# Performance work log

Measured on AMD Instinct MI355X. Metric: run time of the kernel, lower is better.

## Reference

```python
import jax, jax.numpy as jnp
import numpy as np

MEAN_DEG = 3.8
QS = (2, 4, 8, 16, 32, 64)
POOL_DIM = 100
BP_ITERS = 10


def _bn(x, g, b):
    # BatchNorm1d in training mode: biased batch statistics over the node dim
    m = x.mean(0)
    v = ((x - m) ** 2).mean(0)
    return g * (x - m) * jax.lax.rsqrt(v + 1e-5) + b


def _gcn_sparse(x, src, dst, n, w, b):
    # GCNConv: add self loops, symmetric deg^-1/2 normalization, scatter-add aggregation
    loop = jnp.arange(n, dtype=src.dtype)
    s2 = jnp.concatenate([src, loop])
    d2 = jnp.concatenate([dst, loop])
    deg = jax.ops.segment_sum(jnp.ones(s2.shape[0], x.dtype), d2, num_segments=n)
    dinv = jnp.where(deg > 0, jax.lax.rsqrt(deg), 0.0)
    norm = (dinv[s2] * dinv[d2])[:, None]
    return jax.ops.segment_sum((x @ w)[s2] * norm, d2, num_segments=n) + b


def _gcn_dense(x, adj, w, b):
    # GCN on the dense pooled adjacency (pooled graphs are fully connected)
    n = adj.shape[-1]
    A = adj + jnp.eye(n, dtype=adj.dtype)
    d = A.sum(-1)
    dinv = jnp.where(d > 0, jax.lax.rsqrt(d), 0.0)
    An = dinv[:, :, None] * A * dinv[:, None, :]
    return jnp.einsum('bij,bjd->bid', An, x @ w) + b


def _bp(src, dst, n, q, beta, seed):
    # SBM-style belief propagation: iterate node marginals psi [n,q] for a fixed
    # number of sweeps; coupling exp(beta), global external field ~ mean_degree.
    key = jax.random.fold_in(jax.random.key(42), seed)
    psi0 = jax.nn.softmax(jax.random.normal(key, (n, q), jnp.float32), -1)
    eb = jnp.expm1(beta)

    def step(psi, _):
        msg = jax.ops.segment_sum(jnp.log1p(eb * psi[src]), dst, num_segments=n)
        field = (MEAN_DEG * beta / n) * psi.sum(0)
        return jax.nn.softmax(msg - field, -1), None

    psi, _ = jax.lax.scan(step, psi0, None, length=BP_ITERS)
    return psi


def _forward(x, w11, b11, g11, be11, w12, b12, g12, be12, w13, b13, g13, be13,
             bp_betas, pool_w, pool_b,
             w21, b21, g21, be21, w22, b22, g22, be22, w23, b23, g23, be23,
             fc1_w, fc1_b, fc2_w, fc2_b, edge_index, num_graphs):
    n = x.shape[0]
    B = num_graphs
    N = n // B
    src, dst = edge_index[0], edge_index[1]
    # per-graph dense adjacency (edge_index_to_csr -> todense, duplicates sum)
    adj = jnp.zeros((B, N, N), x.dtype).at[src // N, src % N, dst % N].add(1.0)

    # stage 1: three GCN + BN layers on the raw graph
    x11 = _bn(_gcn_sparse(x, src, dst, n, w11, b11), g11, be11)
    x12 = _bn(_gcn_sparse(x11, src, dst, n, w12, b12), g12, be12)
    x13 = _bn(_gcn_sparse(x12, src, dst, n, w13, b13), g13, be13)
    x1_out = jnp.concatenate([x11, x12, x13], -1).reshape(B, N, -1).max(1)  # [B,90]

    # six belief-propagation runs -> concat assignments [n, 2+4+...+64 = 126]
    s1 = jnp.concatenate([_bp(src, dst, n, q, bp_betas[i], i) for i, q in enumerate(QS)], -1)
    s1 = s1 @ pool_w + pool_b  # [n, 100]

    # dense diff-pool
    s1 = jax.nn.softmax(s1.reshape(B, N, POOL_DIM), -1)
    p1_x = jnp.einsum('bnk,bnd->bkd', s1, x13.reshape(B, N, -1))   # [B,100,30]
    p1_adj = jnp.einsum('bnk,bnm,bml->bkl', s1, adj, s1)           # [B,100,100]

    # stage 2: three dense GCN + BN layers on pooled graphs
    C = 30
    x21 = _bn(_gcn_dense(p1_x, p1_adj, w21, b21).reshape(-1, C), g21, be21)
    x22 = _bn(_gcn_dense(x21.reshape(B, POOL_DIM, C), p1_adj, w22, b22).reshape(-1, C), g22, be22)
    x23 = _bn(_gcn_dense(x22.reshape(B, POOL_DIM, C), p1_adj, w23, b23).reshape(-1, C), g23, be23)
    x2_out = jnp.concatenate([x21, x22, x23], -1).reshape(B, POOL_DIM, -1).max(1)  # [B,90]

    conv_out = jnp.concatenate([x1_out, x2_out], -1)  # [B,180]
    out = jax.nn.relu(conv_out @ fc1_w + fc1_b) @ fc2_w + fc2_b  # dropout p=0 -> identity
    return out, jnp.zeros((1,), x.dtype)


def setup_inputs() -> dict:
    key = jax.random.key(0)
    B, N, EP = 64, 1024, 8192
    ks = jax.random.split(key, 24)
    x = jax.random.normal(ks[0], (B * N, 3), jnp.float32)
    off = (jnp.arange(B, dtype=jnp.int32) * N)[:, None]
    src = (jax.random.randint(ks[1], (B, EP), 0, N, jnp.int32) + off).reshape(-1)
    dst = (jax.random.randint(ks[2], (B, EP), 0, N, jnp.int32) + off).reshape(-1)
    edge_index = jnp.stack([src, dst])

    def lin(k, i, o):
        return jax.random.normal(k, (i, o), jnp.float32) / np.sqrt(i)

    p = {}
    dims1 = [(3, 30), (30, 30), (30, 30)]
    for idx, (i, o) in enumerate(dims1, 1):
        p['w1%d' % idx] = lin(ks[2 + idx], i, o)
        p['b1%d' % idx] = jnp.zeros((o,), jnp.float32)
        p['g1%d' % idx] = jnp.ones((o,), jnp.float32)
        p['be1%d' % idx] = jnp.zeros((o,), jnp.float32)
    for idx in (1, 2, 3):
        p['w2%d' % idx] = lin(ks[8 + idx], 30, 30)
        p['b2%d' % idx] = jnp.zeros((30,), jnp.float32)
        p['g2%d' % idx] = jnp.ones((30,), jnp.float32)
        p['be2%d' % idx] = jnp.zeros((30,), jnp.float32)
    qs = np.array(QS, np.float32)
    p['bp_betas'] = jnp.asarray(np.log(qs / (np.sqrt(MEAN_DEG) - 1.0) + 1.0))
    p['pool_w'] = lin(ks[15], 126, 100); p['pool_b'] = jnp.zeros((100,), jnp.float32)
    p['fc1_w'] = lin(ks[16], 180, 50); p['fc1_b'] = jnp.zeros((50,), jnp.float32)
    p['fc2_w'] = lin(ks[17], 50, 6); p['fc2_b'] = jnp.zeros((6,), jnp.float32)
    return {'x': x, 'edge_index': edge_index, 'num_graphs': B, **p}


def reference(x, edge_index, num_graphs, w11, b11, g11, be11, w12, b12, g12, be12,
              w13, b13, g13, be13, bp_betas, pool_w, pool_b,
              w21, b21, g21, be21, w22, b22, g22, be22, w23, b23, g23, be23,
              fc1_w, fc1_b, fc2_w, fc2_b):
    return _forward(x, w11, b11, g11, be11, w12, b12, g12, be12, w13, b13, g13, be13,
                    bp_betas, pool_w, pool_b,
                    w21, b21, g21, be21, w22, b22, g22, be22, w23, b23, g23, be23,
                    fc1_w, fc1_b, fc2_w, fc2_b, edge_index, num_graphs)
```

## Files before the change

### kernel.cpp

```cpp
#include <hip/hip_runtime.h>
#include <stdint.h>
#include <float.h>


constexpr int NN    = 65536;
constexpr int NEDGE = 524288;
constexpr int NBG   = 64;

__constant__ int cQS[6]   = {2,4,8,16,32,64};

__device__ __forceinline__ void tf2x32(uint32_t k0, uint32_t k1, uint32_t x0, uint32_t x1,
                                       uint32_t& o0, uint32_t& o1){
  uint32_t ks[3] = {k0, k1, k0 ^ k1 ^ 0x1BD11BDAu};
  x0 += ks[0]; x1 += ks[1];
  const int RA[4] = {13,15,26,6}, RB[4] = {17,29,16,24};
  #pragma unroll
  for (int i=0;i<5;i++){
    const int* r = (i&1)? RB : RA;
    #pragma unroll
    for (int j=0;j<4;j++){
      x0 += x1;
      x1 = (x1 << r[j]) | (x1 >> (32 - r[j]));
      x1 ^= x0;
    }
// ... 126 lines not shown
                                              float* __restrict__ h, int nrow){
  __shared__ float ws[CIN*30];
  int t = threadIdx.x;
  for (int i=t;i<CIN*30;i+=256) ws[i] = w[i];
  __syncthreads();
  int id = blockIdx.x*256 + t;
  if (id >= nrow*30) return;
  int v = id/30, j = id - v*30;
  const float* xr = x + v*CIN;
  float acc = 0.f;
  #pragma unroll
  for (int k=0;k<CIN;k++) acc += xr[k]*ws[k*30+j];
  h[id] = acc;
}

__global__ __launch_bounds__(256) void k_mm30c(const float* __restrict__ x, const float* __restrict__ wfold,
                                               const float* __restrict__ cvec, float* __restrict__ h, int nrow){
  __shared__ float ws[900];
  __shared__ float cl[30];
  int t = threadIdx.x;
  for (int i=t;i<900;i+=256) ws[i] = wfold[i];
  if (t < 30) cl[t] = cvec[t];
  __syncthreads();
  int id = blockIdx.x*256 + t;
  if (id >= nrow*30) return;
  int v = id/30, j = id - v*30;
  const float* xr = x + v*30;
  float acc = cl[j];
  #pragma unroll
  for (int k=0;k<30;k++) acc += xr[k]*ws[k*30+j];
  h[id] = acc;
}

__global__ __launch_bounds__(256) void k_gcn_agg(const float* __restrict__ h, const int* __restrict__ rp,
    const int* __restrict__ col, const float* __restrict__ dinv, const float* __restrict__ bias,
    float* __restrict__ y, float* __restrict__ gS, float* __restrict__ gQ){
  __shared__ float binS[30], binQ[30];
  int t = threadIdx.x;
  if (t < 30){ binS[t]=0.f; binQ[t]=0.f; }
  __syncthreads();
  int b = blockIdx.x;
  int xcd = b & 7, i = b >> 3;
  int gs = i/60, j = i - gs*60;
  int graph = gs*8 + xcd;
  int idwg = j*256 + t;
  int rw = idwg/15, pr = idwg - rw*15;
  int v = graph*1024 + rw;
  float dv = dinv[v];
  float accx = 0.f, accy = 0.f;
  int a = rp[v], e = rp[v+1];
  for (; a+4<=e; a+=4){
    int s0=col[a], s1=col[a+1], s2=col[a+2], s3=col[a+3];
    float d0=dinv[s0], d1=dinv[s1], d2=dinv[s2], d3=dinv[s3];
    float2 h0=*(const float2*)(h+s0*30+2*pr), h1=*(const float2*)(h+s1*30+2*pr);
    float2 h2=*(const float2*)(h+s2*30+2*pr), h3=*(const float2*)(h+s3*30+2*pr);
    accx += h0.x*(d0*dv); accy += h0.y*(d0*dv);
    accx += h1.x*(d1*dv); accy += h1.y*(d1*dv);
    accx += h2.x*(d2*dv); accy += h2.y*(d2*dv);
    accx += h3.x*(d3*dv); accy += h3.y*(d3*dv);
  }
  for (; a<e; ++a){
    int s = col[a];
    float w = dinv[s]*dv;
    float2 hv = *(const float2*)(h+s*30+2*pr);
    accx += hv.x*w; accy += hv.y*w;
  }
  float2 hs = *(const float2*)(h + v*30 + 2*pr);
  float w2 = dv*dv;
  accx += hs.x*w2; accy += hs.y*w2;
  float2 o; o.x = accx + bias[2*pr]; o.y = accy + bias[2*pr+1];
  *(float2*)(y + v*30 + 2*pr) = o;
  atomicAdd(&binS[2*pr],   o.x); atomicAdd(&binQ[2*pr],   o.x*o.x);
  atomicAdd(&binS[2*pr+1], o.y); atomicAdd(&binQ[2*pr+1], o.y*o.y);
  __syncthreads();
  if (t < 30){
    int slot = (b & 63)*30 + t;
    atomicAdd(&gS[slot], binS[t]);
    atomicAdd(&gQ[slot], binQ[t]);
  }
}

template<int FOLD>
__global__ __launch_bounds__(256) void k_bnw(float* __restrict__ gS, float* __restrict__ gQ, float n,
    const float* __restrict__ g, const float* __restrict__ be,
    const float* __restrict__ wnext, float* __restrict__ sfc,
    float* __restrict__ wfold, float* __restrict__ cvec){
  __shared__ float s_l[30], c_l[30];
  int t = threadIdx.x;
  if (t < 30){
    float s=0.f, q=0.f;
    for (int u=0;u<64;u++){ s += gS[u*30+t]; q += gQ[u*30+t]; }
    float m = s/n;
    float var = q/n - m*m;
    float sc = g[t]*(1.0f/sqrtf(var+1e-5f));
    float c0 = be[t] - sc*m;
    s_l[t]=sc; c_l[t]=c0;
    sfc[t]=sc; sfc[32+t]=c0;
    for (int u=0;u<64;u++){ gS[u*30+t]=0.f; gQ[u*30+t]=0.f; }
  }
  __syncthreads();
  if (FOLD){
    for (int i=t;i<900;i+=256) wfold[i] = s_l[i/30]*wnext[i];
    if (t<30){
      float c=0.f;
      for (int k=0;k<30;k++) c += c_l[k]*wnext[k*30+t];
      cvec[t]=c;
    }
  }
}

__device__ __forceinline__ void bp_decode2(int b, int& graph, int& run, int& jj){
  int xcd = b & 7, i = b >> 3;
  int gs = i >> 7, j = i & 127;
  if      (j <   4){ run=0; jj=j;    }
// ... 58 lines not shown
    float m0=fmaxf(z[0],z[1]), m1=fmaxf(z[1],z[0]);
    float e0=expf(z[0]-m0), e1=expf(z[1]-m1);
    float s0=e0+e1, s1=e1+e0;
    float p0=e0/s0, p1=e1/s1;
    ((float2*)(psi_pk + (size_t)NN*CO))[row] = make_float2(p0,p1);
    ((float2*)(lg     + (size_t)NN*CO))[row] = make_float2(log1pf(eb*p0), log1pf(eb*p1));
  } else {
    int rw = idx >> L2T, ct = idx & (TPR-1);
    int row = graph*1024 + rw;
    float z[4];
    #pragma unroll
    for (int r=0;r<4;r++){
      uint32_t b0,b1;
      tf2x32(k0,k1, 0u, (uint32_t)(row*Q + 4*ct + r), b0,b1);
      uint32_t bits = b0 ^ b1;
      float f = __uint_as_float((bits>>9) | 0x3F800000u) - 1.0f;
      const float lo = __uint_as_float(0xBF7FFFFFu);
      float u = fmaxf(lo, f*2.0f + lo);
      z[r] = __uint_as_float(0x3FB504F3u) * erfinv32(u);
    }
    float m0=z[0],m1=z[1],m2=z[2],m3=z[3];
    bfly_max4<TPR>(m0,m1,m2,m3);
    float e0=expf(z[0]-m0), e1=expf(z[1]-m1), e2=expf(z[2]-m2), e3=expf(z[3]-m3);
    float s0=e0,s1=e1,s2=e2,s3=e3;
    bfly_sum4<TPR>(s0,s1,s2,s3);
    float p0=e0/s0, p1=e1/s1, p2=e2/s2, p3=e3/s3;
    ((float4*)(psi_pk + (size_t)NN*CO))[(size_t)row*TPR + ct] = make_float4(p0,p1,p2,p3);
    ((float4*)(lg     + (size_t)NN*CO))[(size_t)row*TPR + ct] =
        make_float4(log1pf(eb*p0), log1pf(eb*p1), log1pf(eb*p2), log1pf(eb*p3));
  }
}

__global__ __launch_bounds__(256) void k_bp_first(float* __restrict__ psi_pk, float* __restrict__ lg,
                                                  const float* __restrict__ betas){
  int graph, run, jj;
  bp_decode2(blockIdx.x, graph, run, jj);
  uint32_t k0, k1;
  tf2x32(0u, 42u, 0u, (uint32_t)run, k0, k1);
  float eb = expm1f(betas[run]);
  switch(run){
    case 0: bp_first_elem2< 2, 0, 1,0>(graph, jj, psi_pk, lg, eb, k0, k1); break;
    case 1: bp_first_elem2< 4, 2, 1,0>(graph, jj, psi_pk, lg, eb, k0, k1); break;
    case 2: bp_first_elem2< 8, 6, 2,1>(graph, jj, psi_pk, lg, eb, k0, k1); break;
    case 3: bp_first_elem2<16,14, 4,2>(graph, jj, psi_pk, lg, eb, k0, k1); break;
    case 4: bp_first_elem2<32,30, 8,3>(graph, jj, psi_pk, lg, eb, k0, k1); break;
    default:bp_first_elem2<64,62,16,4>(graph, jj, psi_pk, lg, eb, k0, k1); break;
  }
}

template<int Q, int CO, int TPR, int L2T>
__device__ __forceinline__ void bp_step_elem2(int graph, int run, int jj,
    const float* __restrict__ lcur, float* __restrict__ nxt, float* __restrict__ lnxt,
    const int* __restrict__ rp, const int* __restrict__ col,
    const float* __restrict__ field, float eb, int fin){
  int idx = jj*256 + (int)threadIdx.x;
  if constexpr (Q == 2){
    int row = graph*1024 + idx;
    const float2* B2 = (const float2*)(lcur + (size_t)NN*CO);
    float a0=0.f, a1=0.f;
    int a = rp[row], b2 = rp[row+1];
    for (; a+8<=b2; a+=8){
      int s0=col[a],s1=col[a+1],s2=col[a+2],s3=col[a+3];
      int s4=col[a+4],s5=col[a+5],s6=col[a+6],s7=col[a+7];
      float2 u0=B2[s0], u1=B2[s1], u2=B2[s2], u3=B2[s3];
      float2 u4=B2[s4], u5=B2[s5], u6=B2[s6], u7=B2[s7];
      a0+=u0.x; a1+=u0.y; a0+=u1.x; a1+=u1.y;
      a0+=u2.x; a1+=u2.y; a0+=u3.x; a1+=u3.y;
// ... 47 lines not shown
      float4 u0=B4[(size_t)s0*TPR+ct], u1=B4[(size_t)s1*TPR+ct];
      float4 u2=B4[(size_t)s2*TPR+ct], u3=B4[(size_t)s3*TPR+ct];
      a0+=u0.x; a1+=u0.y; a2+=u0.z; a3+=u0.w;
      a0+=u1.x; a1+=u1.y; a2+=u1.z; a3+=u1.w;
      a0+=u2.x; a1+=u2.y; a2+=u2.z; a3+=u2.w;
      a0+=u3.x; a1+=u3.y; a2+=u3.z; a3+=u3.w;
    }
    for (; a<b2; ++a){
      float4 u = B4[(size_t)col[a]*TPR+ct];
      a0+=u.x; a1+=u.y; a2+=u.z; a3+=u.w;
    }
    const float4 fld = *(const float4*)(field + run*64 + 4*ct);
    float v0 = a0 - fld.x, v1 = a1 - fld.y, v2 = a2 - fld.z, v3 = a3 - fld.w;
    float m0=v0,m1=v1,m2=v2,m3=v3;
    bfly_max4<TPR>(m0,m1,m2,m3);
    float e0=expf(v0-m0), e1=expf(v1-m1), e2=expf(v2-m2), e3=expf(v3-m3);
    float s0=e0,s1=e1,s2=e2,s3=e3;
    bfly_sum4<TPR>(s0,s1,s2,s3);
    float p0=e0/s0, p1=e1/s1, p2=e2/s2, p3=e3/s3;
    if (fin){
      float* o = nxt + (size_t)row*126 + CO + 4*ct;
      o[0]=p0; o[1]=p1; o[2]=p2; o[3]=p3;
    } else {
      ((float4*)(nxt  + (size_t)NN*CO))[(size_t)row*TPR+ct] = make_float4(p0,p1,p2,p3);
      ((float4*)(lnxt + (size_t)NN*CO))[(size_t)row*TPR+ct] =
          make_float4(log1pf(eb*p0), log1pf(eb*p1), log1pf(eb*p2), log1pf(eb*p3));
    }
  }
}

__global__ __launch_bounds__(256) void k_bp_step(
    float* __restrict__ nxt, const float* __restrict__ lcur, float* __restrict__ lnxt,
    const int* __restrict__ rp, const int* __restrict__ col,
    const float* __restrict__ field, const float* __restrict__ betas, int fin){
  int graph, run, jj;
  bp_decode2(blockIdx.x, graph, run, jj);
  float eb = expm1f(betas[run]);
  switch(run){
    case 0: bp_step_elem2< 2, 0, 1,0>(graph, run, jj, lcur, nxt, lnxt, rp, col, field, eb, fin); break;
    case 1: bp_step_elem2< 4, 2, 1,0>(graph, run, jj, lcur, nxt, lnxt, rp, col, field, eb, fin); break;
    case 2: bp_step_elem2< 8, 6, 2,1>(graph, run, jj, lcur, nxt, lnxt, rp, col, field, eb, fin); break;
    case 3: bp_step_elem2<16,14, 4,2>(graph, run, jj, lcur, nxt, lnxt, rp, col, field, eb, fin); break;
    case 4: bp_step_elem2<32,30, 8,3>(graph, run, jj, lcur, nxt, lnxt, rp, col, field, eb, fin); break;
    default:bp_step_elem2<64,62,16,4>(graph, run, jj, lcur, nxt, lnxt, rp, col, field, eb, fin); break;
  }
}

__global__ __launch_bounds__(64) void k_colsum_part(const float* __restrict__ psi_pk, float* __restrict__ part){
  int b = blockIdx.x;
  int xcd = b & 7, i = b >> 3;
  int gs = i/24, rem = i - gs*24;
  int run = rem >> 2, cg = rem & 3;
  int graph = gs*8 + xcd;
  int chunk = graph*4 + cg;
  int q = cQS[run];
  int co = (run==0)?0:(run==1)?2:(run==2)?6:(run==3)?14:(run==4)?30:62;
  int c = threadIdx.x;
  if (q >= 4){
    int nq = q >> 2;
    if (c >= nq) return;
    const float4* p4 = (const float4*)(psi_pk + (size_t)NN*co + (size_t)chunk*256*q) + c;
    float s0=0.f,s1=0.f,s2=0.f,s3=0.f;
    #pragma unroll 8
    for (int r=0;r<256;r++){
      float4 u = p4[(size_t)r*nq];
      s0+=u.x; s1+=u.y; s2+=u.z; s3+=u.w;
    }
    float* o = part + (run*256 + chunk)*64 + 4*c;
    o[0]=s0; o[1]=s1; o[2]=s2; o[3]=s3;
  } else {
    if (c >= q) return;
    float s = 0.f;
    const float* p = psi_pk + (size_t)NN*co + (size_t)chunk*256*q + c;
    #pragma unroll 8
    for (int r=0;r<256;r++) s += p[r*q];
    part[(run*256 + chunk)*64 + c] = s;
  }
}

__global__ void k_field(const float* __restrict__ part, const float* __restrict__ betas,
                        float* __restrict__ field){
  int id = threadIdx.x;
  int run = id >> 6, c = id & 63;
  if (c >= cQS[run]) return;
  float s = 0.f;
  for (int b=0;b<256;b++) s += part[(run*256 + b)*64 + c];
  float beta = betas[run];
  field[id] = s * (3.8f*beta/65536.0f);
}

__global__ __launch_bounds__(256) void k_catT(const float* __restrict__ cat, float* __restrict__ catT){
  __shared__ float tile[64*127];
  int b = blockIdx.x, t = threadIdx.x;
  const float* src = cat + (size_t)b*64*126;
  for (int i=t;i<8064;i+=256){
    int r = i/126, k = i - r*126;
    tile[r*127 + k] = src[i];
  }
  __syncthreads();
  for (int i=t;i<8064;i+=256){
    int k = i>>6, r = i&63;
    catT[(size_t)k*65536 + b*64 + r] = tile[r*127 + k];
  }
}

__global__ __launch_bounds__(256) void k_s1t(const float* __restrict__ catT, const float* __restrict__ pw,
                                             const float* __restrict__ pb, float* __restrict__ s1){
  __shared__ float wl[12600];
  __shared__ float pbl[100];
  __shared__ float redM[2][128];
  __shared__ float redS[2][128];
  int t = threadIdx.x;
  for (int i=t;i<12600;i+=256) wl[i] = pw[i];
  if (t < 100) pbl[t] = pb[t];
// ... 49 lines not shown
  int a = rp[v], e = rp[v+1];
  for (; a+8<=e; a+=8){
    int s0=col[a], s1_=col[a+1], s2=col[a+2], s3=col[a+3];
    int s4=col[a+4], s5=col[a+5], s6=col[a+6], s7=col[a+7];
    float4 u0=S4[(size_t)s0*25+quad], u1=S4[(size_t)s1_*25+quad];
    float4 u2=S4[(size_t)s2*25+quad], u3=S4[(size_t)s3*25+quad];
    float4 u4=S4[(size_t)s4*25+quad], u5=S4[(size_t)s5*25+quad];
    float4 u6=S4[(size_t)s6*25+quad], u7=S4[(size_t)s7*25+quad];
    a0+=u0.x; a1+=u0.y; a2+=u0.z; a3+=u0.w;
    a0+=u1.x; a1+=u1.y; a2+=u1.z; a3+=u1.w;
    a0+=u2.x; a1+=u2.y; a2+=u2.z; a3+=u2.w;
    a0+=u3.x; a1+=u3.y; a2+=u3.z; a3+=u3.w;
    a0+=u4.x; a1+=u4.y; a2+=u4.z; a3+=u4.w;
    a0+=u5.x; a1+=u5.y; a2+=u5.z; a3+=u5.w;
    a0+=u6.x; a1+=u6.y; a2+=u6.z; a3+=u6.w;
    a0+=u7.x; a1+=u7.y; a2+=u7.z; a3+=u7.w;
  }
  for (; a+4<=e; a+=4){
    int s0=col[a], s1_=col[a+1], s2=col[a+2], s3=col[a+3];
    float4 u0=S4[(size_t)s0*25+quad], u1=S4[(size_t)s1_*25+quad];
    float4 u2=S4[(size_t)s2*25+quad], u3=S4[(size_t)s3*25+quad];
    a0+=u0.x; a1+=u0.y; a2+=u0.z; a3+=u0.w;
    a0+=u1.x; a1+=u1.y; a2+=u1.z; a3+=u1.w;
    a0+=u2.x; a1+=u2.y; a2+=u2.z; a3+=u2.w;
    a0+=u3.x; a1+=u3.y; a2+=u3.z; a3+=u3.w;
  }
  for (; a<e; ++a){
    float4 u = S4[(size_t)col[a]*25+quad];
    a0+=u.x; a1+=u.y; a2+=u.z; a3+=u.w;
  }
  ((float4*)T)[(size_t)v*25 + quad] = make_float4(a0,a1,a2,a3);
}

__global__ __launch_bounds__(512) void k_p1adj_sk(const float* __restrict__ s1, const float* __restrict__ T,
                                                  float* __restrict__ part){
  __shared__ float sS[6400];
  __shared__ float sT[6400];
  int blk = blockIdx.x;
  int b = blk >> 2, qtr = blk & 3;
  int t = threadIdx.x;
  int tk = t/20, tl = t - tk*20;
  bool act = t < 500;
  int k0 = tk*4, l0 = tl*5;
  float acc[4][5];
  #pragma unroll
  for (int i=0;i<4;i++)
    #pragma unroll
    for (int j=0;j<5;j++) acc[i][j] = 0.f;
  const float* s1b = s1 + (size_t)b*102400;
  const float* Tb  = T  + (size_t)b*102400;
  for (int c=qtr*4; c<qtr*4+4; c++){
    for (int i=t;i<6400;i+=512){ sS[i] = s1b[c*6400+i]; sT[i] = Tb[c*6400+i]; }
    __syncthreads();
    if (act){
      #pragma unroll 2
      for (int n=0;n<64;n++){
        const float* sr = &sS[n*100 + k0];
        const float* tr = &sT[n*100 + l0];
        float s0=sr[0], s1v=sr[1], s2=sr[2], s3=sr[3];
        float t0=tr[0], t1=tr[1], t2=tr[2], t3=tr[3], t4=tr[4];
        acc[0][0]+=s0*t0; acc[0][1]+=s0*t1; acc[0][2]+=s0*t2; acc[0][3]+=s0*t3; acc[0][4]+=s0*t4;
        acc[1][0]+=s1v*t0; acc[1][1]+=s1v*t1; acc[1][2]+=s1v*t2; acc[1][3]+=s1v*t3; acc[1][4]+=s1v*t4;
        acc[2][0]+=s2*t0; acc[2][1]+=s2*t1; acc[2][2]+=s2*t2; acc[2][3]+=s2*t3; acc[2][4]+=s2*t4;
        acc[3][0]+=s3*t0; acc[3][1]+=s3*t1; acc[3][2]+=s3*t2; acc[3][3]+=s3*t3; acc[3][4]+=s3*t4;
      }
    }
    __syncthreads();
  }
  if (act){
    float* pp = part + (size_t)qtr*640000 + (size_t)b*10000;
    #pragma unroll
    for (int i=0;i<4;i++){
      float* o = pp + (k0+i)*100 + l0;
      #pragma unroll
      for (int j=0;j<5;j++) o[j] = acc[i][j];
    }
  }
}

__global__ __launch_bounds__(256) void k_p1x_sk(const float* __restrict__ s1, const float* __restrict__ y3,
                                                const float* __restrict__ sfc, float* __restrict__ part){
  __shared__ float sS[6400];
  __shared__ float sX[1920];
  int blk = blockIdx.x;
  int b = blk >> 2, qtr = blk & 3;
  int t = threadIdx.x;
  int tk = t/10, tl = t - tk*10;
  bool act = t < 250;
  int k0 = tk*4, d0 = tl*3;
  float acc[4][3];
  #pragma unroll
  for (int i=0;i<4;i++)
    #pragma unroll
    for (int j=0;j<3;j++) acc[i][j] = 0.f;
  const float* s1b = s1 + (size_t)b*102400;
  const float* xb  = y3 + (size_t)b*30720;
  for (int c=qtr*4; c<qtr*4+4; c++){
    for (int i=t;i<6400;i+=256) sS[i] = s1b[c*6400+i];
    for (int i=t;i<1920;i+=256){
      int f = i % 30;
      sX[i] = sfc[f]*xb[c*1920+i] + sfc[32+f];
    }
    __syncthreads();
    if (act){
      #pragma unroll 2
      for (int n=0;n<64;n++){
        const float* sr = &sS[n*100 + k0];
        const float* xr = &sX[n*30 + d0];
        float s0=sr[0], s1v=sr[1], s2=sr[2], s3=sr[3];
        float x0=xr[0], x1=xr[1], x2=xr[2];
        acc[0][0]+=s0*x0; acc[0][1]+=s0*x1; acc[0][2]+=s0*x2;
        acc[1][0]+=s1v*x0; acc[1][1]+=s1v*x1; acc[1][2]+=s1v*x2;
        acc[2][0]+=s2*x0; acc[2][1]+=s2*x1; acc[2][2]+=s2*x2;
        acc[3][0]+=s3*x0; acc[3][1]+=s3*x1; acc[3][2]+=s3*x2;
      }
    }
    __syncthreads();
  }
  if (act){
    float* pp = part + (size_t)qtr*192000 + (size_t)b*3000;
    #pragma unroll
    for (int i=0;i<4;i++){
      float* o = pp + (k0+i)*30 + d0;
      #pragma unroll
      for (int j=0;j<3;j++) o[j] = acc[i][j];
    }
  }
}

__global__ __launch_bounds__(256) void k_ppred(const float* __restrict__ partA, const float* __restrict__ partX,
                                               float* __restrict__ padj, float* __restrict__ px){
  int id = blockIdx.x*256 + threadIdx.x;
  if (id < 640000){
    float s = partA[id] + partA[640000+id] + partA[1280000+id] + partA[1920000+id];
    padj[id] = s;
  } else if (id < 832000){
    int j = id - 640000;
    float s = partX[j] + partX[192000+j] + partX[384000+j] + partX[576000+j];
    px[j] = s;
  }
}

__global__ __launch_bounds__(256) void k_An1(const float* __restrict__ padj, float* __restrict__ An){
  __shared__ float dv[100];
  int b = blockIdx.x, t = threadIdx.x;
  if (t < 100){
    const float* r = padj + (size_t)b*10000 + t*100;
    float s = 0.f;
    for (int l=0;l<100;l++){
      float v = r[l];
      if (l==t) v += 1.0f;
      s += v;
    }
    dv[t] = 1.0f/sqrtf(s);
  }
  __syncthreads();
  for (int i=t;i<10000;i+=256){
    int k = i/100, l = i - k*100;
    float a = padj[(size_t)b*10000 + i] + ((k==l)? 1.0f : 0.0f);
    An[(size_t)b*10000 + i] = (dv[k]*a)*dv[l];
  }
}

__global__ __launch_bounds__(256) void k_y2(const float* __restrict__ An, const float* __restrict__ h,
    const float* __restrict__ bias, float* __restrict__ y,
    float* __restrict__ gS, float* __restrict__ gQ){
  __shared__ float binS[30], binQ[30];
  int t = threadIdx.x;
  if (t < 30){ binS[t]=0.f; binQ[t]=0.f; }
  __syncthreads();
  int id = blockIdx.x*256 + t;
  float val = 0.f;
  int d = 0;
  if (id < NBG*100*30){
    d = id % 30;
    int bk = id / 30;
    int b = bk / 100;
    const float* Ar = An + bk*100;
    const float* hb = h + b*100*30;
    float acc = 0.f;
    for (int l=0;l<100;l++) acc += Ar[l]*hb[l*30+d];
    val = acc + bias[d];
    y[id] = val;
    atomicAdd(&binS[d], val);
    atomicAdd(&binQ[d], val*val);
  }
  __syncthreads();
  if (t < 30){
    int slot = (blockIdx.x & 63)*30 + t;
    atomicAdd(&gS[slot], binS[t]);
    atomicAdd(&gQ[slot], binQ[t]);
  }
}

__global__ __launch_bounds__(256) void k_pool2(const float* __restrict__ A,
    const float* __restrict__ Bv, const float* __restrict__ Cv,
    const float* __restrict__ sfcBase,
    int rows, float* __restrict__ conv, int coff){
  __shared__ float lds[256*31];
  int b = blockIdx.x, a = blockIdx.y, t = threadIdx.x;
  const float* X = (a==0)? A : ((a==1)? Bv : Cv);
  const float* sf = sfcBase + a*64;
  float acc[30];
  #pragma unroll
  for (int f=0;f<30;f++) acc[f] = -FLT_MAX;
  for (int r=t; r<rows; r+=256){
    const float* xr = X + (size_t)(b*rows + r)*30;
    #pragma unroll
    for (int f=0;f<30;f++) acc[f] = fmaxf(acc[f], sf[f]*xr[f] + sf[32+f]);
  }
  #pragma unroll
  for (int f=0;f<30;f++) lds[t*31+f] = acc[f];
  __syncthreads();
  for (int s=128;s>0;s>>=1){
    if (t<s){
// ... 50 lines not shown
  uint8_t* basep = (uint8_t*)d_ws;
  size_t off = 0;
  auto take = [&](size_t bytes)->void*{
    void* p = basep + off;
    off = (off + bytes + 255) & ~(size_t)255;
    return p;
  };
  int* degi    = (int*)take((size_t)NN*4);
  int* dego    = (int*)take((size_t)NN*4);
  int* cntA    = (int*)take((size_t)NN*4);
  int* cntB    = (int*)take((size_t)NN*4);
  float* gS    = (float*)take(64*30*4);
  float* gQ    = (float*)take(64*30*4);
  int* rp_in   = (int*)take((size_t)(NN+1)*4);
  int* rp_out  = (int*)take((size_t)(NN+1)*4);
  int* bsum    = (int*)take(512*4);
  int* col_in  = (int*)take((size_t)NEDGE*4);
  int* col_out = (int*)take((size_t)NEDGE*4);
  float* dinv  = (float*)take((size_t)NN*4);
  float* hbuf  = (float*)take((size_t)NN*30*4);
  float* X1    = (float*)take((size_t)NN*30*4);
  float* X2    = (float*)take((size_t)NN*30*4);
  float* X3    = (float*)take((size_t)NN*30*4);
  float* bufA  = (float*)take((size_t)NN*126*4);
  float* bufB  = (float*)take((size_t)NN*126*4);
  float* logA  = (float*)take((size_t)NN*126*4);
  float* logB  = (float*)take((size_t)NN*126*4);
  float* partCS= (float*)take((size_t)6*256*64*4);
  float* fieldv= (float*)take(384*4);
  float* sfcAll= (float*)take(6*64*4);
  float* wfold = (float*)take(960*4);
  float* cvec  = (float*)take(32*4);
  float* px    = (float*)take(192000*4);
  float* padj  = (float*)take(640000*4);
  float* An    = (float*)take(640000*4);
  float* h2    = (float*)take(192000*4);
  float* X21   = (float*)take(192000*4);
  float* X22   = (float*)take(192000*4);
  float* X23   = (float*)take(192000*4);
  float* conv  = (float*)take(64*180*4);

  float* catT     = logA;
  float* pAdjPart = logB;
  float* pPxPart  = logB + 2560000;

  hipMemsetAsync(degi, 0, (size_t)4*NN*4 + 2*64*30*4, stream);
  k_count<<<2048,256,0,stream>>>(src,dst,degi,dego);
  k_scan1<<<dim3(256,2),256,0,stream>>>(degi, dego, rp_in, rp_out, bsum);
  k_scan2<<<2,256,0,stream>>>(bsum);
  k_scan3<<<dim3(256,2),256,0,stream>>>(rp_in, rp_out, bsum);
  k_fill<<<dim3(2048,2),256,0,stream>>>(src, dst, rp_in, rp_out, cntA, cntB, col_in, col_out);
  k_sortrow<<<dim3(256,2),256,0,stream>>>(rp_in, rp_out, col_in, col_out, src, dst, degi, dinv);

  k_mm30<3><<<7680,256,0,stream>>>(x, w11, hbuf, NN);
  k_gcn_agg<<<3840,256,0,stream>>>(hbuf, rp_in, col_in, dinv, b11, X1, gS, gQ);
  k_bnw<1><<<1,256,0,stream>>>(gS, gQ, 65536.f, g11, be11, w12, sfcAll+0*64, wfold, cvec);
  k_mm30c<<<7680,256,0,stream>>>(X1, wfold, cvec, hbuf, NN);
  k_gcn_agg<<<3840,256,0,stream>>>(hbuf, rp_in, col_in, dinv, b12, X2, gS, gQ);
  k_bnw<1><<<1,256,0,stream>>>(gS, gQ, 65536.f, g12, be12, w13, sfcAll+1*64, wfold, cvec);
  k_mm30c<<<7680,256,0,stream>>>(X2, wfold, cvec, hbuf, NN);
  k_gcn_agg<<<3840,256,0,stream>>>(hbuf, rp_in, col_in, dinv, b13, X3, gS, gQ);
  k_bnw<0><<<1,256,0,stream>>>(gS, gQ, 65536.f, g13, be13, nullptr, sfcAll+2*64, nullptr, nullptr);
  k_pool2<<<dim3(NBG,3),256,0,stream>>>(X1, X2, X3, sfcAll, 1024, conv, 0);

  k_bp_first<<<8192,256,0,stream>>>(bufA, logA, betas);
  float* cur = bufA;  float* nxt = bufB;
  float* lcur = logA; float* lnxt = logB;
  for (int it=0; it<10; ++it){
    k_colsum_part<<<1536,64,0,stream>>>(cur, partCS);
    k_field<<<1,384,0,stream>>>(partCS, betas, fieldv);
    int fin = (it==9);
    k_bp_step<<<8192,256,0,stream>>>(nxt, lcur, lnxt, rp_in, col_in, fieldv, betas, fin);
    float* tp = cur;  cur = nxt;   nxt = tp;
    float* tl = lcur; lcur = lnxt; lnxt = tl;
  }

  k_catT<<<1024,256,0,stream>>>(bufA, catT);
  k_s1t<<<512,256,0,stream>>>(catT, poolw, poolb, bufB);
  k_T<<<6400,256,0,stream>>>(bufB, rp_out, col_out, bufA);
  k_p1adj_sk<<<256,512,0,stream>>>(bufB, bufA, pAdjPart);
  k_p1x_sk<<<256,256,0,stream>>>(bufB, X3, sfcAll+2*64, pPxPart);
  k_ppred<<<3250,256,0,stream>>>(pAdjPart, pPxPart, padj, px);
  k_An1<<<64,256,0,stream>>>(padj, An);

  k_mm30<30><<<750,256,0,stream>>>(px, w21, h2, NBG*100);
  k_y2<<<750,256,0,stream>>>(An, h2, b21, X21, gS, gQ);
  k_bnw<1><<<1,256,0,stream>>>(gS, gQ, 6400.f, g21, be21, w22, sfcAll+3*64, wfold, cvec);
  k_mm30c<<<750,256,0,stream>>>(X21, wfold, cvec, h2, NBG*100);
  k_y2<<<750,256,0,stream>>>(An, h2, b22, X22, gS, gQ);
  k_bnw<1><<<1,256,0,stream>>>(gS, gQ, 6400.f, g22, be22, w23, sfcAll+4*64, wfold, cvec);
  k_mm30c<<<750,256,0,stream>>>(X22, wfold, cvec, h2, NBG*100);
  k_y2<<<750,256,0,stream>>>(An, h2, b23, X23, gS, gQ);
  k_bnw<0><<<1,256,0,stream>>>(gS, gQ, 6400.f, g23, be23, nullptr, sfcAll+5*64, nullptr, nullptr);
  k_pool2<<<dim3(NBG,3),256,0,stream>>>(X21, X22, X23, sfcAll+3*64, 100, conv, 90);

  k_fc<<<64,64,0,stream>>>(conv, fc1w, fc1b, fc2w, fc2b, out);
}
```

Measured before the change: 1.288 ms.

## Overlap first-stage GCN layers with BP sweeps via auxiliary blocks in shared launches

Moves the independent first-stage GCN work (linear transforms, sparse aggregation, BN statistics folding and max-pooling) into extra blocks appended to the BP kernel launches, so those stages run alongside the BP iterations instead of as separate serial launches. The BN fold is carried as a second block of k_field. The pooled-adjacency and pooled-feature partial GEMMs are merged into one launch, and the partial-sum reduction is fused with the An normalisation. This cuts launch count and serial dependency chains, at the cost of heavier, divergent kernels with more shared memory and a hand-tracked dependency schedule across iterations.

Result: faster. 1.235 ms, median of 2 (-4.1%).

```diff
diff --git a/kernel.cpp b/kernel.cpp
--- a/kernel.cpp
+++ b/kernel.cpp
@@ -182,54 +182,6 @@
   h[id] = acc;
 }
 
-__global__ __launch_bounds__(256) void k_gcn_agg(const float* __restrict__ h, const int* __restrict__ rp,
-    const int* __restrict__ col, const float* __restrict__ dinv, const float* __restrict__ bias,
-    float* __restrict__ y, float* __restrict__ gS, float* __restrict__ gQ){
-  __shared__ float binS[30], binQ[30];
-  int t = threadIdx.x;
-  if (t < 30){ binS[t]=0.f; binQ[t]=0.f; }
-  __syncthreads();
-  int b = blockIdx.x;
-  int xcd = b & 7, i = b >> 3;
-  int gs = i/60, j = i - gs*60;
-  int graph = gs*8 + xcd;
-  int idwg = j*256 + t;
-  int rw = idwg/15, pr = idwg - rw*15;
-  int v = graph*1024 + rw;
-  float dv = dinv[v];
-  float accx = 0.f, accy = 0.f;
-  int a = rp[v], e = rp[v+1];
-  for (; a+4<=e; a+=4){
-    int s0=col[a], s1=col[a+1], s2=col[a+2], s3=col[a+3];
-    float d0=dinv[s0], d1=dinv[s1], d2=dinv[s2], d3=dinv[s3];
-    float2 h0=*(const float2*)(h+s0*30+2*pr), h1=*(const float2*)(h+s1*30+2*pr);
-    float2 h2=*(const float2*)(h+s2*30+2*pr), h3=*(const float2*)(h+s3*30+2*pr);
-    accx += h0.x*(d0*dv); accy += h0.y*(d0*dv);
-    accx += h1.x*(d1*dv); accy += h1.y*(d1*dv);
-    accx += h2.x*(d2*dv); accy += h2.y*(d2*dv);
-    accx += h3.x*(d3*dv); accy += h3.y*(d3*dv);
-  }
-  for (; a<e; ++a){
-    int s = col[a];
-    float w = dinv[s]*dv;
-    float2 hv = *(const float2*)(h+s*30+2*pr);
-    accx += hv.x*w; accy += hv.y*w;
-  }
-  float2 hs = *(const float2*)(h + v*30 + 2*pr);
-  float w2 = dv*dv;
-  accx += hs.x*w2; accy += hs.y*w2;
-  float2 o; o.x = accx + bias[2*pr]; o.y = accy + bias[2*pr+1];
-  *(float2*)(y + v*30 + 2*pr) = o;
-  atomicAdd(&binS[2*pr],   o.x); atomicAdd(&binQ[2*pr],   o.x*o.x);
-  atomicAdd(&binS[2*pr+1], o.y); atomicAdd(&binQ[2*pr+1], o.y*o.y);
-  __syncthreads();
-  if (t < 30){
-    int slot = (b & 63)*30 + t;
-    atomicAdd(&gS[slot], binS[t]);
-    atomicAdd(&gQ[slot], binQ[t]);
-  }
-}
-
 template<int FOLD>
 __global__ __launch_bounds__(256) void k_bnw(float* __restrict__ gS, float* __restrict__ gQ, float n,
     const float* __restrict__ g, const float* __restrict__ be,
@@ -354,7 +306,25 @@
 }
 
 __global__ __launch_bounds__(256) void k_bp_first(float* __restrict__ psi_pk, float* __restrict__ lg,
-                                                  const float* __restrict__ betas){
+                                                  const float* __restrict__ betas,
+                                                  const float* __restrict__ xin,
+                                                  const float* __restrict__ w11,
+                                                  float* __restrict__ hbuf){
+  if (blockIdx.x >= 8192){
+    __shared__ float ws[90];
+    int t = threadIdx.x;
+    for (int i=t;i<90;i+=256) ws[i] = w11[i];
+    __syncthreads();
+    int id = ((int)blockIdx.x - 8192)*256 + t;
+    if (id >= NN*30) return;
+    int v = id/30, j = id - v*30;
+    const float* xr = xin + v*3;
+    float acc = 0.f;
+    #pragma unroll
+    for (int k=0;k<3;k++) acc += xr[k]*ws[k*30+j];
+    hbuf[id] = acc;
+    return;
+  }
   int graph, run, jj;
   bp_decode2(blockIdx.x, graph, run, jj);
   uint32_t k0, k1;
@@ -468,7 +438,101 @@
 __global__ __launch_bounds__(256) void k_bp_step(
     float* __restrict__ nxt, const float* __restrict__ lcur, float* __restrict__ lnxt,
     const int* __restrict__ rp, const int* __restrict__ col,
-    const float* __restrict__ field, const float* __restrict__ betas, int fin){
+    const float* __restrict__ field, const float* __restrict__ betas, int fin,
+    int auxType, const float* __restrict__ aA, const float* __restrict__ aB,
+    const float* __restrict__ aC, float* __restrict__ aO,
+    float* __restrict__ agS, float* __restrict__ agQ,
+    const float* __restrict__ adinv, const float* __restrict__ asfc,
+    float* __restrict__ aconv){
+  if (blockIdx.x >= 8192){
+    __shared__ float smem[960];
+    int ab = (int)blockIdx.x - 8192;
+    int t = threadIdx.x;
+    if (auxType == 1){
+      float* binS = smem; float* binQ = smem + 32;
+      if (t < 30){ binS[t]=0.f; binQ[t]=0.f; }
+      __syncthreads();
+      int xcd = ab & 7, i = ab >> 3;
+      int gs = i/60, j = i - gs*60;
+      int graph = gs*8 + xcd;
+      int idwg = j*256 + t;
+      int rw = idwg/15, pr = idwg - rw*15;
+      int v = graph*1024 + rw;
+      float dv = adinv[v];
+      float accx = 0.f, accy = 0.f;
+      int a = rp[v], e = rp[v+1];
+      for (; a+4<=e; a+=4){
+        int s0=col[a], s1=col[a+1], s2=col[a+2], s3=col[a+3];
+        float d0=adinv[s0], d1=adinv[s1], d2=adinv[s2], d3=adinv[s3];
+        float2 h0=*(const float2*)(aA+s0*30+2*pr), h1=*(const float2*)(aA+s1*30+2*pr);
+        float2 h2=*(const float2*)(aA+s2*30+2*pr), h3=*(const float2*)(aA+s3*30+2*pr);
+        accx += h0.x*(d0*dv); accy += h0.y*(d0*dv);
+        accx += h1.x*(d1*dv); accy += h1.y*(d1*dv);
+        accx += h2.x*(d2*dv); accy += h2.y*(d2*dv);
+        accx += h3.x*(d3*dv); accy += h3.y*(d3*dv);
+      }
+      for (; a<e; ++a){
+        int s = col[a];
+        float w = adinv[s]*dv;
+        float2 hv = *(const float2*)(aA+s*30+2*pr);
+        accx += hv.x*w; accy += hv.y*w;
+      }
+      float2 hs = *(const float2*)(aA + v*30 + 2*pr);
+      float w2 = dv*dv;
+      accx += hs.x*w2; accy += hs.y*w2;
+      float2 o; o.x = accx + aB[2*pr]; o.y = accy + aB[2*pr+1];
+      *(float2*)(aO + v*30 + 2*pr) = o;
+      atomicAdd(&binS[2*pr],   o.x); atomicAdd(&binQ[2*pr],   o.x*o.x);
+      atomicAdd(&binS[2*pr+1], o.y); atomicAdd(&binQ[2*pr+1], o.y*o.y);
+      __syncthreads();
+      if (t < 30){
+        int slot = (ab & 63)*30 + t;
+        atomicAdd(&agS[slot], binS[t]);
+        atomicAdd(&agQ[slot], binQ[t]);
+      }
+    } else if (auxType == 2){
+      float* ws = smem; float* cl = smem + 904;
+      for (int i=t;i<900;i+=256) ws[i] = aB[i];
+      if (t < 30) cl[t] = aC[t];
+      __syncthreads();
+      int id = ab*256 + t;
+      if (id < NN*30){
+        int v = id/30, j = id - v*30;
+        const float* xr = aA + v*30;
+        float acc = cl[j];
+        #pragma unroll
+        for (int k=0;k<30;k++) acc += xr[k]*ws[k*30+j];
+        aO[id] = acc;
+      }
+    } else if (auxType == 3){
+      int b2 = ab & 63, a = ab >> 6;
+      const float* X = (a==0)? aA : ((a==1)? aB : aC);
+      const float* sf = asfc + a*64;
+      float acc[30];
+      #pragma unroll
+      for (int f=0;f<30;f++) acc[f] = -FLT_MAX;
+      for (int r=t; r<1024; r+=256){
+        const float* xr = X + (size_t)(b2*1024 + r)*30;
+        #pragma unroll
+        for (int f=0;f<30;f++) acc[f] = fmaxf(acc[f], sf[f]*xr[f] + sf[32+f]);
+      }
+      #pragma unroll
+      for (int off=32; off; off>>=1){
+        #pragma unroll
+        for (int f=0;f<30;f++) acc[f] = fmaxf(acc[f], __shfl_xor(acc[f], off, 64));
+      }
+      int w = t>>6, lane = t&63;
+      if (lane == 0){
+        #pragma unroll
+        for (int f=0;f<30;f++) smem[w*30+f] = acc[f];
+      }
+      __syncthreads();
+      if (t < 30)
+        aconv[b2*180 + a*30 + t] =
+          fmaxf(fmaxf(smem[t], smem[30+t]), fmaxf(smem[60+t], smem[90+t]));
+    }
+    return;
+  }
   int graph, run, jj;
   bp_decode2(blockIdx.x, graph, run, jj);
   float eb = expm1f(betas[run]);
@@ -515,7 +579,37 @@
 }
 
 __global__ void k_field(const float* __restrict__ part, const float* __restrict__ betas,
-                        float* __restrict__ field){
+                        float* __restrict__ field,
+                        int auxFold, float* __restrict__ gS, float* __restrict__ gQ, float n,
+                        const float* __restrict__ g, const float* __restrict__ be,
+                        const float* __restrict__ wnext, float* __restrict__ sfc,
+                        float* __restrict__ wfold, float* __restrict__ cvec){
+  if (blockIdx.x == 1){
+    if (auxFold < 0) return;
+    __shared__ float s_l[30], c_l[30];
+    int t = threadIdx.x;
+    if (t < 30){
+      float s=0.f, q=0.f;
+      for (int u=0;u<64;u++){ s += gS[u*30+t]; q += gQ[u*30+t]; }
+      float m = s/n;
+      float var = q/n - m*m;
+      float sc = g[t]*(1.0f/sqrtf(var+1e-5f));
+      float c0 = be[t] - sc*m;
+      s_l[t]=sc; c_l[t]=c0;
+      sfc[t]=sc; sfc[32+t]=c0;
+      for (int u=0;u<64;u++){ gS[u*30+t]=0.f; gQ[u*30+t]=0.f; }
+    }
+    __syncthreads();
+    if (auxFold == 1){
+      for (int i=t;i<900;i+=384) wfold[i] = s_l[i/30]*wnext[i];
+      if (t<30){
+        float c=0.f;
+        for (int k=0;k<30;k++) c += c_l[k]*wnext[k*30+t];
+        cvec[t]=c;
+      }
+    }
+    return;
+  }
   int id = threadIdx.x;
   int run = id >> 6, c = id & 63;
   if (c >= cQS[run]) return;
@@ -631,133 +725,130 @@
   ((float4*)T)[(size_t)v*25 + quad] = make_float4(a0,a1,a2,a3);
 }
 
-__global__ __launch_bounds__(512) void k_p1adj_sk(const float* __restrict__ s1, const float* __restrict__ T,
-                                                  float* __restrict__ part){
+__global__ __launch_bounds__(512) void k_p1ax(const float* __restrict__ s1, const float* __restrict__ T,
+                                              const float* __restrict__ y3, const float* __restrict__ sfc,
+                                              float* __restrict__ partA, float* __restrict__ partX){
   __shared__ float sS[6400];
   __shared__ float sT[6400];
-  int blk = blockIdx.x;
-  int b = blk >> 2, qtr = blk & 3;
   int t = threadIdx.x;
-  int tk = t/20, tl = t - tk*20;
-  bool act = t < 500;
-  int k0 = tk*4, l0 = tl*5;
-  float acc[4][5];
-  #pragma unroll
-  for (int i=0;i<4;i++)
+  if (blockIdx.x < 256){
+    int blk = blockIdx.x;
+    int b = blk >> 2, qtr = blk & 3;
+    int tk = t/20, tl = t - tk*20;
+    bool act = t < 500;
+    int k0 = tk*4, l0 = tl*5;
+    float acc[4][5];
     #pragma unroll
-    for (int j=0;j<5;j++) acc[i][j] = 0.f;
-  const float* s1b = s1 + (size_t)b*102400;
-  const float* Tb  = T  + (size_t)b*102400;
-  for (int c=qtr*4; c<qtr*4+4; c++){
-    for (int i=t;i<6400;i+=512){ sS[i] = s1b[c*6400+i]; sT[i] = Tb[c*6400+i]; }
+    for (int i=0;i<4;i++)
+      #pragma unroll
+      for (int j=0;j<5;j++) acc[i][j] = 0.f;
+    const float* s1b = s1 + (size_t)b*102400;
+    const float* Tb  = T  + (size_t)b*102400;
+    for (int c=qtr*4; c<qtr*4+4; c++){
+      for (int i=t;i<6400;i+=512){ sS[i] = s1b[c*6400+i]; sT[i] = Tb[c*6400+i]; }
+      __syncthreads();
+      if (act){
+        #pragma unroll 2
+        for (int n=0;n<64;n++){
+          const float* sr = &sS[n*100 + k0];
+          const float* tr = &sT[n*100 + l0];
+          float s0=sr[0], s1v=sr[1], s2=sr[2], s3=sr[3];
+          float t0=tr[0], t1=tr[1], t2=tr[2], t3=tr[3], t4=tr[4];
+          acc[0][0]+=s0*t0; acc[0][1]+=s0*t1; acc[0][2]+=s0*t2; acc[0][3]+=s0*t3; acc[0][4]+=s0*t4;
+          acc[1][0]+=s1v*t0; acc[1][1]+=s1v*t1; acc[1][2]+=s1v*t2; acc[1][3]+=s1v*t3; acc[1][4]+=s1v*t4;
+          acc[2][0]+=s2*t0; acc[2][1]+=s2*t1; acc[2][2]+=s2*t2; acc[2][3]+=s2*t3; acc[2][4]+=s2*t4;
+          acc[3][0]+=s3*t0; acc[3][1]+=s3*t1; acc[3][2]+=s3*t2; acc[3][3]+=s3*t3; acc[3][4]+=s3*t4;
+        }
+      }
+      __syncthreads();
+    }
+    if (act){
+      float* pp = partA + (size_t)qtr*640000 + (size_t)b*10000;
+      #pragma unroll
+      for (int i=0;i<4;i++){
+        float* o = pp + (k0+i)*100 + l0;
+        #pragma unroll
+        for (int j=0;j<5;j++) o[j] = acc[i][j];
+      }
+    }
+  } else {
+    int blk = blockIdx.x - 256;
+    int b = blk >> 2, qtr = blk & 3;
+    float* sX = sT;
+    int tk = t/10, tl = t - tk*10;
+    bool act = t < 250;
+    int k0 = tk*4, d0 = tl*3;
+    float acc[4][3];
+    #pragma unroll
+    for (int i=0;i<4;i++)
+      #pragma unroll
+      for (int j=0;j<3;j++) acc[i][j] = 0.f;
+    const float* s1b = s1 + (size_t)b*102400;
+    const float* xb  = y3 + (size_t)b*30720;
+    for (int c=qtr*4; c<qtr*4+4; c++){
+      for (int i=t;i<6400;i+=512) sS[i] = s1b[c*6400+i];
+      for (int i=t;i<1920;i+=512){
+        int f = i % 30;
+        sX[i] = sfc[f]*xb[c*1920+i] + sfc[32+f];
+      }
+      __syncthreads();
+      if (act){
+        #pragma unroll 2
+        for (int n=0;n<64;n++){
+          const float* sr = &sS[n*100 + k0];
+          const float* xr = &sX[n*30 + d0];
+          float s0=sr[0], s1v=sr[1], s2=sr[2], s3=sr[3];
+          float x0=xr[0], x1=xr[1], x2=xr[2];
+          acc[0][0]+=s0*x0; acc[0][1]+=s0*x1; acc[0][2]+=s0*x2;
+          acc[1][0]+=s1v*x0; acc[1][1]+=s1v*x1; acc[1][2]+=s1v*x2;
+          acc[2][0]+=s2*x0; acc[2][1]+=s2*x1; acc[2][2]+=s2*x2;
+          acc[3][0]+=s3*x0; acc[3][1]+=s3*x1; acc[3][2]+=s3*x2;
+        }
+      }
+      __syncthreads();
+    }
+    if (act){
+      float* pp = partX + (size_t)qtr*192000 + (size_t)b*3000;
+      #pragma unroll
+      for (int i=0;i<4;i++){
+        float* o = pp + (k0+i)*30 + d0;
+        #pragma unroll
+        for (int j=0;j<3;j++) o[j] = acc[i][j];
+      }
+    }
+  }
+}
+
+__global__ __launch_bounds__(256) void k_anpx(const float* __restrict__ pA, const float* __restrict__ pX,
+                                              float* __restrict__ An, float* __restrict__ px){
+  if (blockIdx.x < 64){
+    __shared__ float pj[10000];
+    __shared__ float dv[100];
+    int b = blockIdx.x, t = threadIdx.x;
+    size_t base = (size_t)b*10000;
+    for (int i=t;i<10000;i+=256)
+      pj[i] = pA[base+i] + pA[640000+base+i] + pA[1280000+base+i] + pA[1920000+base+i];
     __syncthreads();
-    if (act){
-      #pragma unroll 2
-      for (int n=0;n<64;n++){
-        const float* sr = &sS[n*100 + k0];
-        const float* tr = &sT[n*100 + l0];
-        float s0=sr[0], s1v=sr[1], s2=sr[2], s3=sr[3];
-        float t0=tr[0], t1=tr[1], t2=tr[2], t3=tr[3], t4=tr[4];
-        acc[0][0]+=s0*t0; acc[0][1]+=s0*t1; acc[0][2]+=s0*t2; acc[0][3]+=s0*t3; acc[0][4]+=s0*t4;
-        acc[1][0]+=s1v*t0; acc[1][1]+=s1v*t1; acc[1][2]+=s1v*t2; acc[1][3]+=s1v*t3; acc[1][4]+=s1v*t4;
-        acc[2][0]+=s2*t0; acc[2][1]+=s2*t1; acc[2][2]+=s2*t2; acc[2][3]+=s2*t3; acc[2][4]+=s2*t4;
-        acc[3][0]+=s3*t0; acc[3][1]+=s3*t1; acc[3][2]+=s3*t2; acc[3][3]+=s3*t3; acc[3][4]+=s3*t4;
-      }
+    if (t < 100){
+      const float* r = pj + t*100;
+      float s = 0.f;
+      for (int l=0;l<100;l++){
+        float v = r[l];
+        if (l==t) v += 1.0f;
+        s += v;
+      }
+      dv[t] = 1.0f/sqrtf(s);
     }
     __syncthreads();
-  }
-  if (act){
-    float* pp = part + (size_t)qtr*640000 + (size_t)b*10000;
-    #pragma unroll
-    for (int i=0;i<4;i++){
-      float* o = pp + (k0+i)*100 + l0;
-      #pragma unroll
-      for (int j=0;j<5;j++) o[j] = acc[i][j];
-    }
-  }
-}
-
-__global__ __launch_bounds__(256) void k_p1x_sk(const float* __restrict__ s1, const float* __restrict__ y3,
-                                                const float* __restrict__ sfc, float* __restrict__ part){
-  __shared__ float sS[6400];
-  __shared__ float sX[1920];
-  int blk = blockIdx.x;
-  int b = blk >> 2, qtr = blk & 3;
-  int t = threadIdx.x;
-  int tk = t/10, tl = t - tk*10;
-  bool act = t < 250;
-  int k0 = tk*4, d0 = tl*3;
-  float acc[4][3];
-  #pragma unroll
-  for (int i=0;i<4;i++)
-    #pragma unroll
-    for (int j=0;j<3;j++) acc[i][j] = 0.f;
-  const float* s1b = s1 + (size_t)b*102400;
-  const float* xb  = y3 + (size_t)b*30720;
-  for (int c=qtr*4; c<qtr*4+4; c++){
-    for (int i=t;i<6400;i+=256) sS[i] = s1b[c*6400+i];
-    for (int i=t;i<1920;i+=256){
-      int f = i % 30;
-      sX[i] = sfc[f]*xb[c*1920+i] + sfc[32+f];
-    }
-    __syncthreads();
-    if (act){
-      #pragma unroll 2
-      for (int n=0;n<64;n++){
-        const float* sr = &sS[n*100 + k0];
-        const float* xr = &sX[n*30 + d0];
-        float s0=sr[0], s1v=sr[1], s2=sr[2], s3=sr[3];
-        float x0=xr[0], x1=xr[1], x2=xr[2];
-        acc[0][0]+=s0*x0; acc[0][1]+=s0*x1; acc[0][2]+=s0*x2;
-        acc[1][0]+=s1v*x0; acc[1][1]+=s1v*x1; acc[1][2]+=s1v*x2;
-        acc[2][0]+=s2*x0; acc[2][1]+=s2*x1; acc[2][2]+=s2*x2;
-        acc[3][0]+=s3*x0; acc[3][1]+=s3*x1; acc[3][2]+=s3*x2;
-      }
-    }
-    __syncthreads();
-  }
-  if (act){
-    float* pp = part + (size_t)qtr*192000 + (size_t)b*3000;
-    #pragma unroll
-    for (int i=0;i<4;i++){
-      float* o = pp + (k0+i)*30 + d0;
-      #pragma unroll
-      for (int j=0;j<3;j++) o[j] = acc[i][j];
-    }
-  }
-}
-
-__global__ __launch_bounds__(256) void k_ppred(const float* __restrict__ partA, const float* __restrict__ partX,
-                                               float* __restrict__ padj, float* __restrict__ px){
-  int id = blockIdx.x*256 + threadIdx.x;
-  if (id < 640000){
-    float s = partA[id] + partA[640000+id] + partA[1280000+id] + partA[1920000+id];
-    padj[id] = s;
-  } else if (id < 832000){
-    int j = id - 640000;
-    float s = partX[j] + partX[192000+j] + partX[384000+j] + partX[576000+j];
-    px[j] = s;
-  }
-}
-
-__global__ __launch_bounds__(256) void k_An1(const float* __restrict__ padj, float* __restrict__ An){
-  __shared__ float dv[100];
-  int b = blockIdx.x, t = threadIdx.x;
-  if (t < 100){
-    const float* r = padj + (size_t)b*10000 + t*100;
-    float s = 0.f;
-    for (int l=0;l<100;l++){
-      float v = r[l];
-      if (l==t) v += 1.0f;
-      s += v;
-    }
-    dv[t] = 1.0f/sqrtf(s);
-  }
-  __syncthreads();
-  for (int i=t;i<10000;i+=256){
-    int k = i/100, l = i - k*100;
-    float a = padj[(size_t)b*10000 + i] + ((k==l)? 1.0f : 0.0f);
-    An[(size_t)b*10000 + i] = (dv[k]*a)*dv[l];
+    for (int i=t;i<10000;i+=256){
+      int k = i/100, l = i - k*100;
+      float a = pj[i] + ((k==l)? 1.0f : 0.0f);
+      An[base + i] = (dv[k]*a)*dv[l];
+    }
+  } else {
+    int id = ((int)blockIdx.x - 64)*256 + threadIdx.x;
+    if (id < 192000)
+      px[id] = pX[id] + pX[192000+id] + pX[384000+id] + pX[576000+id];
   }
 }
 
@@ -769,17 +860,15 @@
   if (t < 30){ binS[t]=0.f; binQ[t]=0.f; }
   __syncthreads();
   int id = blockIdx.x*256 + t;
-  float val = 0.f;
-  int d = 0;
   if (id < NBG*100*30){
-    d = id % 30;
+    int d = id % 30;
     int bk = id / 30;
     int b = bk / 100;
     const float* Ar = An + bk*100;
     const float* hb = h + b*100*30;
     float acc = 0.f;
     for (int l=0;l<100;l++) acc += Ar[l]*hb[l*30+d];
-    val = acc + bias[d];
+    float val = acc + bias[d];
     y[id] = val;
     atomicAdd(&binS[d], val);
     atomicAdd(&binQ[d], val*val);
@@ -896,7 +985,6 @@
   float* wfold = (float*)take(960*4);
   float* cvec  = (float*)take(32*4);
   float* px    = (float*)take(192000*4);
-  float* padj  = (float*)take(640000*4);
   float* An    = (float*)take(640000*4);
   float* h2    = (float*)take(192000*4);
   float* X21   = (float*)take(192000*4);
@@ -916,25 +1004,30 @@
   k_fill<<<dim3(2048,2),256,0,stream>>>(src, dst, rp_in, rp_out, cntA, cntB, col_in, col_out);
   k_sortrow<<<dim3(256,2),256,0,stream>>>(rp_in, rp_out, col_in, col_out, src, dst, degi, dinv);
 
-  k_mm30<3><<<7680,256,0,stream>>>(x, w11, hbuf, NN);
-  k_gcn_agg<<<3840,256,0,stream>>>(hbuf, rp_in, col_in, dinv, b11, X1, gS, gQ);
-  k_bnw<1><<<1,256,0,stream>>>(gS, gQ, 65536.f, g11, be11, w12, sfcAll+0*64, wfold, cvec);
-  k_mm30c<<<7680,256,0,stream>>>(X1, wfold, cvec, hbuf, NN);
-  k_gcn_agg<<<3840,256,0,stream>>>(hbuf, rp_in, col_in, dinv, b12, X2, gS, gQ);
-  k_bnw<1><<<1,256,0,stream>>>(gS, gQ, 65536.f, g12, be12, w13, sfcAll+1*64, wfold, cvec);
-  k_mm30c<<<7680,256,0,stream>>>(X2, wfold, cvec, hbuf, NN);
-  k_gcn_agg<<<3840,256,0,stream>>>(hbuf, rp_in, col_in, dinv, b13, X3, gS, gQ);
-  k_bnw<0><<<1,256,0,stream>>>(gS, gQ, 65536.f, g13, be13, nullptr, sfcAll+2*64, nullptr, nullptr);
-  k_pool2<<<dim3(NBG,3),256,0,stream>>>(X1, X2, X3, sfcAll, 1024, conv, 0);
-
-  k_bp_first<<<8192,256,0,stream>>>(bufA, logA, betas);
+  k_bp_first<<<15872,256,0,stream>>>(bufA, logA, betas, x, w11, hbuf);
+
   float* cur = bufA;  float* nxt = bufB;
   float* lcur = logA; float* lnxt = logB;
   for (int it=0; it<10; ++it){
     k_colsum_part<<<1536,64,0,stream>>>(cur, partCS);
-    k_field<<<1,384,0,stream>>>(partCS, betas, fieldv);
+    int fold = (it==1||it==3)? 1 : ((it==5)? 0 : -1);
+    const float* gg = (it==1)? g11 : ((it==3)? g12 : g13);
+    const float* bb = (it==1)? be11: ((it==3)? be12: be13);
+    const float* wn = (it==1)? w12 : ((it==3)? w13 : nullptr);
+    float* sfc = (it==1)? sfcAll : ((it==3)? sfcAll+64 : sfcAll+128);
+    k_field<<<2,384,0,stream>>>(partCS, betas, fieldv, fold, gS, gQ, 65536.f,
+                                gg, bb, wn, sfc, wfold, cvec);
     int fin = (it==9);
-    k_bp_step<<<8192,256,0,stream>>>(nxt, lcur, lnxt, rp_in, col_in, fieldv, betas, fin);
+    int auxType = 0, auxN = 0;
+    const float *aA=nullptr, *aB=nullptr, *aC=nullptr; float *aO=nullptr;
+    if      (it==0){ auxType=1; auxN=3840; aA=hbuf; aB=b11; aO=X1; }
+    else if (it==1){ auxType=2; auxN=7680; aA=X1; aB=wfold; aC=cvec; aO=hbuf; }
+    else if (it==2){ auxType=1; auxN=3840; aA=hbuf; aB=b12; aO=X2; }
+    else if (it==3){ auxType=2; auxN=7680; aA=X2; aB=wfold; aC=cvec; aO=hbuf; }
+    else if (it==4){ auxType=1; auxN=3840; aA=hbuf; aB=b13; aO=X3; }
+    else if (it==5){ auxType=3; auxN=192;  aA=X1; aB=X2; aC=X3; }
+    k_bp_step<<<8192+auxN,256,0,stream>>>(nxt, lcur, lnxt, rp_in, col_in, fieldv, betas, fin,
+        auxType, aA, aB, aC, aO, gS, gQ, dinv, sfcAll, conv);
     float* tp = cur;  cur = nxt;   nxt = tp;
     float* tl = lcur; lcur = lnxt; lnxt = tl;
   }
@@ -942,10 +1035,8 @@
   k_catT<<<1024,256,0,stream>>>(bufA, catT);
   k_s1t<<<512,256,0,stream>>>(catT, poolw, poolb, bufB);
   k_T<<<6400,256,0,stream>>>(bufB, rp_out, col_out, bufA);
-  k_p1adj_sk<<<256,512,0,stream>>>(bufB, bufA, pAdjPart);
-  k_p1x_sk<<<256,256,0,stream>>>(bufB, X3, sfcAll+2*64, pPxPart);
-  k_ppred<<<3250,256,0,stream>>>(pAdjPart, pPxPart, padj, px);
-  k_An1<<<64,256,0,stream>>>(padj, An);
+  k_p1ax<<<512,512,0,stream>>>(bufB, bufA, X3, sfcAll+128, pAdjPart, pPxPart);
+  k_anpx<<<814,256,0,stream>>>(pAdjPart, pPxPart, An, px);
 
   k_mm30<30><<<750,256,0,stream>>>(px, w21, h2, NBG*100);
   k_y2<<<750,256,0,stream>>>(An, h2, b21, X21, gS, gQ);
```
